# Kernel tuning notes

Measured on AMD Instinct MI355X. Metric: run time of the kernel, lower is better.

Reference implementation:

```python
import jax, jax.numpy as jnp
import numpy as np

MODS = ['linguistic', 'emotient', 'acoustic', 'image']
HID = {'linguistic': 128, 'emotient': 20, 'acoustic': 64, 'image': 128}
DIMS = {'linguistic': 300, 'emotient': 30, 'acoustic': 88, 'image': 1000}
B, T = 64, 512
TOTAL_HID = sum(HID[m] for m in MODS)  # 340
FUSE_HID = 64


def setup_inputs() -> dict:
    key = jax.random.key(0)
    ks = iter(jax.random.split(key, 64))
    inp = {}
    for mod in MODS:
        H, D = HID[mod], DIMS[mod]
        s = 1.0 / np.sqrt(H)
        inp[f'x_{mod}'] = jax.random.normal(next(ks), (B, T, D), jnp.float32)
        inp[f'present_{mod}'] = jax.random.randint(next(ks), (B, T), 0, 2).astype(jnp.int32)
        inp[f'W_ih_{mod}'] = jax.random.uniform(next(ks), (4 * H, D), jnp.float32, -s, s)
        inp[f'W_hh_{mod}'] = jax.random.uniform(next(ks), (4 * H, H), jnp.float32, -s, s)
        inp[f'b_ih_{mod}'] = jax.random.uniform(next(ks), (4 * H,), jnp.float32, -s, s)
        inp[f'b_hh_{mod}'] = jax.random.uniform(next(ks), (4 * H,), jnp.float32, -s, s)
    inp['seq_length'] = jax.random.randint(next(ks), (B,), 1, T + 1).astype(jnp.int32)
    valid = (jnp.arange(T)[None, :] < inp['seq_length'][:, None])
    inp['lstm_masks'] = valid.astype(jnp.float32)[:, :, None]
    s1 = 1.0 / np.sqrt(TOTAL_HID)
    inp['fuse_W1'] = jax.random.uniform(next(ks), (FUSE_HID, TOTAL_HID), jnp.float32, -s1, s1)
    inp['fuse_b1'] = jax.random.uniform(next(ks), (FUSE_HID,), jnp.float32, -s1, s1)
    s2 = 1.0 / np.sqrt(FUSE_HID)
    inp['fuse_W2'] = jax.random.uniform(next(ks), (1, FUSE_HID), jnp.float32, -s2, s2)
    inp['fuse_b2'] = jax.random.uniform(next(ks), (1,), jnp.float32, -s2, s2)
    return inp


def _lstm_scan(x, present, W_ih, W_hh, b_ih, b_hh):
    # x: [B,T,D], present: [B,T] in {0,1}. Carries (h,c) when not present (async arrival).
    Bn, Tn, _ = x.shape
    H = W_hh.shape[1]
    xg = jnp.einsum('btd,gd->btg', x, W_ih) + b_ih  # [B,T,4H] batched input GEMM

    def step(carry, inp):
        h, c = carry
        xg_t, p_t = inp  # [B,4H], [B]
        g = xg_t + h @ W_hh.T + b_hh
        i, f, gg, o = jnp.split(g, 4, axis=-1)
        i, f, o = jax.nn.sigmoid(i), jax.nn.sigmoid(f), jax.nn.sigmoid(o)
        gg = jnp.tanh(gg)
        c_new = f * c + i * gg
        h_new = o * jnp.tanh(c_new)
        p = p_t[:, None].astype(h.dtype)
        h2 = p * h_new + (1.0 - p) * h
        c2 = p * c_new + (1.0 - p) * c
        return (h2, c2), h2

    init = (jnp.zeros((Bn, H), x.dtype), jnp.zeros((Bn, H), x.dtype))
    _, hs = jax.lax.scan(step, init, (jnp.swapaxes(xg, 0, 1), present.T))
    return jnp.swapaxes(hs, 0, 1)  # [B,T,H]


def reference(x_linguistic, x_emotient, x_acoustic, x_image,
              present_linguistic, present_emotient, present_acoustic, present_image,
              W_ih_linguistic, W_hh_linguistic, b_ih_linguistic, b_hh_linguistic,
              W_ih_emotient, W_hh_emotient, b_ih_emotient, b_hh_emotient,
              W_ih_acoustic, W_hh_acoustic, b_ih_acoustic, b_hh_acoustic,
              W_ih_image, W_hh_image, b_ih_image, b_hh_image,
              seq_length, lstm_masks, fuse_W1, fuse_b1, fuse_W2, fuse_b2):
    xs = {'linguistic': x_linguistic, 'emotient': x_emotient, 'acoustic': x_acoustic, 'image': x_image}
    pres = {'linguistic': present_linguistic, 'emotient': present_emotient,
            'acoustic': present_acoustic, 'image': present_image}
    Wih = {'linguistic': W_ih_linguistic, 'emotient': W_ih_emotient, 'acoustic': W_ih_acoustic, 'image': W_ih_image}
    Whh = {'linguistic': W_hh_linguistic, 'emotient': W_hh_emotient, 'acoustic': W_hh_acoustic, 'image': W_hh_image}
    bih = {'linguistic': b_ih_linguistic, 'emotient': b_ih_emotient, 'acoustic': b_ih_acoustic, 'image': b_ih_image}
    bhh = {'linguistic': b_hh_linguistic, 'emotient': b_hh_emotient, 'acoustic': b_hh_acoustic, 'image': b_hh_image}
    hs = [_lstm_scan(xs[m], pres[m], Wih[m], Whh[m], bih[m], bhh[m]) for m in MODS]
    h = jnp.concatenate(hs, axis=-1)  # [B,T,340]
    # padded timesteps past seq_length are zeros in the original (zeros appended)
    valid = (jnp.arange(h.shape[1])[None, :] < seq_length[:, None]).astype(h.dtype)
    h = h * valid[:, :, None]
    out = h @ fuse_W1.T + fuse_b1  # Dropout is identity at inference
    out = out @ fuse_W2.T + fuse_b2
    return out * lstm_masks
```

## Files before the change

kernel.cpp:

```cpp
#include <hip/hip_runtime.h>
#include <stdint.h>

typedef __bf16 bf16_t;
typedef _Float16 fp16_t;
typedef bf16_t bf16x8 __attribute__((ext_vector_type(8)));
typedef fp16_t fp16x4 __attribute__((ext_vector_type(4)));
typedef float f32x4 __attribute__((ext_vector_type(4)));

#define LOG2E 1.44269504088896340736f

__device__ __forceinline__ float sigm(float x) {
    return __builtin_amdgcn_rcpf(1.f + __builtin_amdgcn_exp2f(-LOG2E * x));
}
__device__ __forceinline__ float tanh_(float x) {
    return 1.f - 2.f * __builtin_amdgcn_rcpf(1.f + __builtin_amdgcn_exp2f((2.f * LOG2E) * x));
}

template <int CTRL>
__device__ __forceinline__ float dpp_add(float x) {
    int perm = __builtin_amdgcn_update_dpp(0, __float_as_int(x), CTRL, 0xF, 0xF, true);
    return x + __int_as_float(perm);
}
__device__ __forceinline__ float red16(float x) {
    x = dpp_add<0xB1>(x);
    x = dpp_add<0x4E>(x);
    x = dpp_add<0x124>(x);
    x = dpp_add<0x128>(x);
    return x;
}

__global__ void prep_fuse(const float* __restrict__ W1, const float* __restrict__ b1,
                          const float* __restrict__ W2, const float* __restrict__ b2,
                          float* __restrict__ v) {
    int u = threadIdx.x;
    if (u < 340) {
        float s = 0.f;
        for (int j = 0; j < 64; j++) s += W2[j] * W1[j * 340 + u];
        v[u] = s;
    } else if (u == 340) {
        float s = 0.f;
        for (int j = 0; j < 64; j++) s += W2[j] * b1[j];
        v[340] = s + b2[0];
    }
}

struct ModGemm {
    const float* x; const float* w; const float* bih; const float* bhh; fp16_t* xg;
    int D; int KB; int N4; int hshift;
};
struct GemmArgs { ModGemm m[4]; int slot_mi[11]; int slot_nb[11]; };

__global__ __launch_bounds__(512) void gemm_all(GemmArgs ga) {
    __shared__ bf16_t sAh[256 * 40];
    __shared__ bf16_t sAl[256 * 40];
    __shared__ bf16_t sB[128 * 40];
    const int slot = blockIdx.y;
    const ModGemm mg = ga.m[ga.slot_mi[slot]];
    const int nb = ga.slot_nb[slot];
    const int ncol0 = nb << 7;
    const int tid = threadIdx.x;
    const int w = tid >> 6, l = tid & 63, lm = l & 15, q = l >> 4;
    const int wm = w & 3, wn = w >> 2;
    const int bm = blockIdx.x;
    const int D = mg.D, N4 = mg.N4;
    const int ra = tid >> 1, ca = (tid & 1) << 4;
    const int rb = tid >> 2, cb = (tid & 3) << 3;

    f32x4 acc[4][4];
#pragma unroll
    for (int a = 0; a < 4; a++)
#pragma unroll
        for (int b = 0; b < 4; b++) acc[a][b] = 0.f;

    for (int kb = 0; kb < mg.KB; kb++) {
        const int k0 = kb << 5;
        {
            long grow = (long)(bm << 8) + ra;
            const float* src = mg.x + grow * D + k0 + ca;
            union { bf16_t e[16]; bf16x8 v[2]; } uh, ul;
            if (k0 + ca + 16 <= D) {
#pragma unroll
                for (int j = 0; j < 16; j += 2) {
                    float2 f = *(const float2*)(src + j);
                    bf16_t h0 = (bf16_t)f.x, h1 = (bf16_t)f.y;
                    uh.e[j] = h0; uh.e[j + 1] = h1;
                    ul.e[j] = (bf16_t)(f.x - (float)h0);
                    ul.e[j + 1] = (bf16_t)(f.y - (float)h1);
                }
            } else {
#pragma unroll
                for (int j = 0; j < 16; j++) {
                    int k = k0 + ca + j;
                    float fv = (k < D) ? mg.x[grow * D + k] : 0.f;
                    bf16_t h0 = (bf16_t)fv;
                    uh.e[j] = h0; ul.e[j] = (bf16_t)(fv - (float)h0);
                }
            }
            *(bf16x8*)&sAh[ra * 40 + ca] = uh.v[0];
            *(bf16x8*)&sAh[ra * 40 + ca + 8] = uh.v[1];
            *(bf16x8*)&sAl[ra * 40 + ca] = ul.v[0];
            *(bf16x8*)&sAl[ra * 40 + ca + 8] = ul.v[1];
        }
        {
            int wrow = ncol0 + rb;
            bool vr = wrow < N4;
            const float* src = mg.w + (long)wrow * D + k0 + cb;
            union { bf16_t e[8]; bf16x8 v; } ub;
            if (vr && (k0 + cb + 8 <= D)) {
#pragma unroll
                for (int j = 0; j < 8; j += 2) {
                    float2 f = *(const float2*)(src + j);
                    ub.e[j] = (bf16_t)f.x; ub.e[j + 1] = (bf16_t)f.y;
                }
            } else {
#pragma unroll
                for (int j = 0; j < 8; j++) {
                    int k = k0 + cb + j;
                    ub.e[j] = (vr && k < D) ? (bf16_t)mg.w[(long)wrow * D + k] : (bf16_t)0.f;
                }
            }
            *(bf16x8*)&sB[rb * 40 + cb] = ub.v;
        }
        __syncthreads();
        bf16x8 ah[4], al[4];
#pragma unroll
        for (int mt = 0; mt < 4; mt++) {
            int row = (wm << 6) + (mt << 4) + lm;
            ah[mt] = *(const bf16x8*)&sAh[row * 40 + (q << 3)];
            al[mt] = *(const bf16x8*)&sAl[row * 40 + (q << 3)];
        }
#pragma unroll
        for (int nt = 0; nt < 4; nt++) {
            bf16x8 bfv = *(const bf16x8*)&sB[((wn << 6) + (nt << 4) + lm) * 40 + (q << 3)];
#pragma unroll
            for (int mt = 0; mt < 4; mt++) {
                acc[mt][nt] = __builtin_amdgcn_mfma_f32_16x16x32_bf16(ah[mt], bfv, acc[mt][nt], 0, 0, 0);
                acc[mt][nt] = __builtin_amdgcn_mfma_f32_16x16x32_bf16(al[mt], bfv, acc[mt][nt], 0, 0, 0);
            }
        }
        __syncthreads();
    }
#pragma unroll
    for (int nt = 0; nt < 4; nt++) {
        int col = ncol0 + (wn << 6) + (nt << 4) + lm;
        if (col >= N4) continue;
        float bias = mg.bih[col] + mg.bhh[col];
        int colout = mg.hshift ? ((col & ((1 << mg.hshift) - 1)) << 2) | (col >> mg.hshift) : col;
#pragma unroll
        for (int mt = 0; mt < 4; mt++) {
#pragma unroll
            for (int r = 0; r < 4; r++) {
                long row = (long)(bm << 8) + (wm << 6) + (mt << 4) + (q << 2) + r;
                int b = (int)(row >> 9), t = (int)(row & 511);
                size_t dst = ((size_t)(t << 6) + b) * N4 + colout;
                mg.xg[dst] = (fp16_t)(acc[mt][nt][r] + bias);
            }
        }
    }
}

struct ModRec {
    const float* whh; const int* present; const fp16_t* xg;
    int N4; int voff;
};
struct RecArgs {
    ModRec m[4];
    const float* vvec;
    float* s_out;
};

template <int H>
__device__ __forceinline__ void rec_step(
    int t, bool act, int w, int lm, int q, int b0,
    const bf16x8 (&wf)[4][H / 32], float vv,
    fp16x4 (&xvs)[4], const fp16_t* const (&px)[4], size_t tstride,
    float (&h_st)[4], float (&c_st)[4],
    const unsigned (&pw)[4], const bf16_t* __restrict__ hbR,
    bf16_t* __restrict__ hbW, float* __restrict__ s_out) {
    constexpr int KT = H / 32, Hp = H + 8;
    if (act) {
        bf16x8 af[KT];
#pragma unroll
        for (int kt = 0; kt < KT; kt++)
            af[kt] = *(const bf16x8*)&hbR[lm * Hp + (kt << 5) + (q << 3)];
        f32x4 accv[4];
#pragma unroll
        for (int g = 0; g < 4; g++)
#pragma unroll
            for (int r = 0; r < 4; r++)
                accv[g][r] = (float)xvs[r][g];
        int tn = t + 4;
        if (tn < 512) {
#pragma unroll
            for (int r = 0; r < 4; r++)
                xvs[r] = *(const fp16x4*)(px[r] + (size_t)tn * tstride);
        }
#pragma unroll
        for (int kt = 0; kt < KT; kt++)
#pragma unroll
            for (int g = 0; g < 4; g++)
                accv[g] = __builtin_amdgcn_mfma_f32_16x16x32_bf16(af[kt], wf[g][kt], accv[g], 0, 0, 0);
        float cr[4];
#pragma unroll
        for (int r = 0; r < 4; r++) {
            float gi = sigm(accv[0][r]);
            float gf = sigm(accv[1][r]);
            float gg = tanh_(accv[2][r]);
            float go = sigm(accv[3][r]);
            float cn = gf * c_st[r] + gi * gg;
            float hn = go * tanh_(cn);
            bool pb = ((pw[r] >> (t & 31)) & 1u) != 0u;
            h_st[r] = pb ? hn : h_st[r];
            c_st[r] = pb ? cn : c_st[r];
            cr[r] = h_st[r] * vv;
        }
        const int u = (w << 4) + lm;
#pragma unroll
        for (int r = 0; r < 4; r++)
            hbW[((q << 2) + r) * Hp + u] = (bf16_t)h_st[r];
#pragma unroll
        for (int r = 0; r < 4; r++)
            cr[r] = red16(cr[r]);
        if (lm == 0) {
#pragma unroll
            for (int r = 0; r < 4; r++)
                s_out[(size_t)((w << 6) + b0 + (q << 2) + r) * 512 + t] = cr[r];
        }
    }
    __syncthreads();
}

template <int H>
__device__ void rec_mfma(const ModRec M, int grp, float* __restrict__ s_out,
                         const float* __restrict__ vvec,
                         unsigned* presw, bf16_t* hb0, bf16_t* hb1, int tid) {
    constexpr int KT = H / 32, TPG = H / 16, Hp = H + 8;
    const int N4 = 4 * H;
    const int w = tid >> 6, l = tid & 63, lm = l & 15, q = l >> 4;
    const int b0 = grp << 4;
    const bool act = (w < TPG);

    for (int i = tid; i < 16 * Hp; i += 512) { hb0[i] = (bf16_t)0.f; hb1[i] = (bf16_t)0.f; }
    for (int i = tid; i < 256; i += 512) {
        const int* ps = M.present + ((b0 + (i >> 4)) << 9) + ((i & 15) << 5);
        unsigned bits = 0u;
#pragma unroll
        for (int j = 0; j < 32; j++) bits |= (unsigned)(ps[j] != 0) << j;
        presw[i] = bits;
    }

    bf16x8 wf[4][KT];
    float vv = 0.f;
    const int u = (w << 4) + lm;
    if (act) {
#pragma unroll
        for (int g = 0; g < 4; g++) {
            int n = g * H + u;
#pragma unroll
            for (int kt = 0; kt < KT; kt++) {
                int k = (kt << 5) + (q << 3);
                const float* sp_ = M.whh + (long)n * H + k;
                float4 f0 = *(const float4*)sp_;
                float4 f1 = *(const float4*)(sp_ + 4);
                union { bf16_t e[8]; bf16x8 v; } uu;
                uu.e[0] = (bf16_t)f0.x; uu.e[1] = (bf16_t)f0.y;
                uu.e[2] = (bf16_t)f0.z; uu.e[3] = (bf16_t)f0.w;
                uu.e[4] = (bf16_t)f1.x; uu.e[5] = (bf16_t)f1.y;
                uu.e[6] = (bf16_t)f1.z; uu.e[7] = (bf16_t)f1.w;
                wf[g][kt] = uu.v;
            }
        }
        vv = vvec[M.voff + u];
    }
    const fp16_t* px[4];
#pragma unroll
    for (int r = 0; r < 4; r++)
        px[r] = M.xg + (size_t)(b0 + (q << 2) + r) * N4 + (u << 2);
    const size_t tstride = (size_t)64 * N4;

    fp16x4 xv[4][4];
    if (act) {
#pragma unroll
        for (int s = 0; s < 4; s++)
#pragma unroll
            for (int r = 0; r < 4; r++)
                xv[s][r] = *(const fp16x4*)(px[r] + (size_t)s * tstride);
    }
    float h_st[4] = {0, 0, 0, 0}, c_st[4] = {0, 0, 0, 0};
    unsigned pw[4] = {0, 0, 0, 0};
    __syncthreads();

    for (int t0 = 0; t0 < 512; t0 += 4) {
        if ((t0 & 31) == 0 && act) {
            int wd = t0 >> 5;
#pragma unroll
            for (int r = 0; r < 4; r++)
                pw[r] = presw[(((q << 2) + r) << 4) + wd];
        }
        rec_step<H>(t0 + 0, act, w, lm, q, b0, wf, vv, xv[0], px, tstride, h_st, c_st, pw, hb0, hb1, s_out);
        rec_step<H>(t0 + 1, act, w, lm, q, b0, wf, vv, xv[1], px, tstride, h_st, c_st, pw, hb1, hb0, s_out);
        rec_step<H>(t0 + 2, act, w, lm, q, b0, wf, vv, xv[2], px, tstride, h_st, c_st, pw, hb0, hb1, s_out);
        rec_step<H>(t0 + 3, act, w, lm, q, b0, wf, vv, xv[3], px, tstride, h_st, c_st, pw, hb1, hb0, s_out);
    }
}

__device__ void rec_emot(const ModRec M, int grp, float* __restrict__ s_out,
                         const float* __restrict__ vvec,
                         float* presf, float* gbuf , float* he , int tid) {
    const int b0 = grp << 4;
    for (int i = tid; i < 16 * 21; i += 512) he[i] = 0.f;
    for (int i = tid; i < 16 * 512; i += 512)
        presf[i] = (float)M.present[((b0 + (i >> 9)) << 9) + (i & 511)];
    const int bl = tid >> 5;
    const int j0 = tid & 31;
    const bool has2 = (j0 < 16);
    float wr0[20], wr1[20], wr2[20];
#pragma unroll
    for (int k = 0; k < 20; k++) {
        wr0[k] = M.whh[j0 * 20 + k];
        wr1[k] = M.whh[(j0 + 32) * 20 + k];
        wr2[k] = has2 ? M.whh[(j0 + 64) * 20 + k] : 0.f;
    }
    const int b2 = tid / 20, u2 = tid % 20;
    const bool p2 = (tid < 320);
    float c_st = 0.f, h_st = 0.f;
    const fp16_t* px = M.xg + (size_t)(b0 + bl) * 80;
    fp16_t e0[4], e1[4], e2[4];
#pragma unroll
    for (int s = 0; s < 4; s++) {
        const fp16_t* p = px + (size_t)s * 5120;
        e0[s] = p[j0]; e1[s] = p[j0 + 32]; e2[s] = has2 ? p[j0 + 64] : (fp16_t)0.f;
    }
    __syncthreads();

    for (int t0 = 0; t0 < 512; t0 += 4) {
#pragma unroll
        for (int s = 0; s < 4; s++) {
            int t = t0 + s;
            float g0 = (float)e0[s];
            float g1 = (float)e1[s];
            float g2 = has2 ? (float)e2[s] : 0.f;
            int tn = t + 4;
            if (tn < 512) {
                const fp16_t* p = px + (size_t)tn * 5120;
                e0[s] = p[j0]; e1[s] = p[j0 + 32]; if (has2) e2[s] = p[j0 + 64];
            }
#pragma unroll
            for (int k = 0; k < 20; k++) {
                float hv = he[bl * 21 + k];
                g0 += wr0[k] * hv; g1 += wr1[k] * hv; g2 += wr2[k] * hv;
            }
            gbuf[bl * 81 + j0] = g0;
            gbuf[bl * 81 + j0 + 32] = g1;
            if (has2) gbuf[bl * 81 + j0 + 64] = g2;
            __syncthreads();
            if (p2) {
                float gi = sigm(gbuf[b2 * 81 + u2]);
                float gf = sigm(gbuf[b2 * 81 + u2 + 20]);
                float gg = tanh_(gbuf[b2 * 81 + u2 + 40]);
                float go = sigm(gbuf[b2 * 81 + u2 + 60]);
                float cn = gf * c_st + gi * gg;
                float hn = go * tanh_(cn);
                float p = presf[b2 * 512 + t];
                bool pb = (p != 0.f);
                h_st = pb ? hn : h_st;
                c_st = pb ? cn : c_st;
                he[b2 * 21 + u2] = h_st;
            }
            __syncthreads();
            if (tid < 16) {
                float ssum = 0.f;
#pragma unroll
                for (int uu = 0; uu < 20; uu++) ssum += he[tid * 21 + uu] * vvec[M.voff + uu];
                s_out[((b0 + tid) << 9) + t] = ssum;
            }
        }
    }
}

__global__ __launch_bounds__(512) void rec_all(RecArgs ra) {
    __shared__ float presf[16 * 512];
    __shared__ bf16_t hb0[16 * 136];
    __shared__ bf16_t hb1[16 * 136];
    __shared__ float gbuf[16 * 81];
    __shared__ float he[16 * 21];
    __shared__ unsigned presw[16 * 16];
    const int tid = threadIdx.x;
    const int bid = blockIdx.x;
    const int mi = bid >> 2, grp = bid & 3;
    const ModRec M = ra.m[mi];
    float* s_out = ra.s_out + (size_t)mi * 8 * 64 * 512;
    if (mi == 1)      rec_emot(M, grp, s_out, ra.vvec, presf, gbuf, he, tid);
    else if (mi == 2) rec_mfma<64>(M, grp, s_out, ra.vvec, presw, hb0, hb1, tid);
    else              rec_mfma<128>(M, grp, s_out, ra.vvec, presw, hb0, hb1, tid);
}

__global__ void fuse_out(const float* __restrict__ sp, const float* __restrict__ v,
                         const float* __restrict__ masks, float* __restrict__ out) {
    int i = threadIdx.x + blockIdx.x * 256;
    float c0 = v[340];
    float s = 0.f;
#pragma unroll
    for (int w = 0; w < 8; w++) s += sp[(size_t)w * 32768 + i];
    s += sp[(size_t)8 * 32768 + i];
#pragma unroll
    for (int w = 16; w < 20; w++) s += sp[(size_t)w * 32768 + i];
#pragma unroll
    for (int w = 24; w < 32; w++) s += sp[(size_t)w * 32768 + i];
    out[i] = masks[i] * (s + c0);
}

extern "C" void kernel_launch(void* const* d_in, const int* in_sizes, int n_in,
                              void* d_out, int out_size, void* d_ws, size_t ws_size,
                              hipStream_t stream) {
    const float* xL = (const float*)d_in[0];
    const int*   pL = (const int*)d_in[1];
    const float* WihL = (const float*)d_in[2];
    const float* WhhL = (const float*)d_in[3];
    const float* bihL = (const float*)d_in[4];
    const float* bhhL = (const float*)d_in[5];
    const float* xE = (const float*)d_in[6];
    const int*   pE = (const int*)d_in[7];
    const float* WihE = (const float*)d_in[8];
    const float* WhhE = (const float*)d_in[9];
    const float* bihE = (const float*)d_in[10];
    const float* bhhE = (const float*)d_in[11];
    const float* xA = (const float*)d_in[12];
    const int*   pA = (const int*)d_in[13];
    const float* WihA = (const float*)d_in[14];
    const float* WhhA = (const float*)d_in[15];
    const float* bihA = (const float*)d_in[16];
    const float* bhhA = (const float*)d_in[17];
    const float* xI = (const float*)d_in[18];
    const int*   pI = (const int*)d_in[19];
    const float* WihI = (const float*)d_in[20];
    const float* WhhI = (const float*)d_in[21];
    const float* bihI = (const float*)d_in[22];
    const float* bhhI = (const float*)d_in[23];
    const float* masks = (const float*)d_in[25];
    const float* fW1 = (const float*)d_in[26];
    const float* fb1 = (const float*)d_in[27];
    const float* fW2 = (const float*)d_in[28];
    const float* fb2 = (const float*)d_in[29];

    char* ws = (char*)d_ws;
    float* v     = (float*)ws;
    float* spart = (float*)(ws + (1 << 16));
    fp16_t* xgL = (fp16_t*)(ws + (1 << 16) + (4 << 20));
    fp16_t* xgE = xgL + (size_t)32768 * 512;
    fp16_t* xgA = xgE + (size_t)32768 * 80;
    fp16_t* xgI = xgA + (size_t)32768 * 256;

    prep_fuse<<<dim3(1), dim3(512), 0, stream>>>(fW1, fb1, fW2, fb2, v);

    GemmArgs ga;
    ga.m[0] = {xL, WihL, bihL, bhhL, xgL, 300,  10, 512, 7};
    ga.m[1] = {xE, WihE, bihE, bhhE, xgE, 30,   1,  80,  0};
    ga.m[2] = {xA, WihA, bihA, bhhA, xgA, 88,   3,  256, 6};
    ga.m[3] = {xI, WihI, bihI, bhhI, xgI, 1000, 32, 512, 7};
    const int mi_tab[11] = {0, 0, 0, 0, 3, 3, 3, 3, 2, 2, 1};
    const int nb_tab[11] = {0, 1, 2, 3, 0, 1, 2, 3, 0, 1, 0};
    for (int i = 0; i < 11; i++) { ga.slot_mi[i] = mi_tab[i]; ga.slot_nb[i] = nb_tab[i]; }
    gemm_all<<<dim3(128, 11), dim3(512), 0, stream>>>(ga);

    RecArgs ra;
    ra.m[0] = {WhhL, pL, xgL, 512, 0};
    ra.m[1] = {WhhE, pE, xgE, 80,  128};
    ra.m[2] = {WhhA, pA, xgA, 256, 148};
    ra.m[3] = {WhhI, pI, xgI, 512, 212};
    ra.vvec = v;
    ra.s_out = spart;
    rec_all<<<dim3(16), dim3(512), 0, stream>>>(ra);

    fuse_out<<<dim3(128), dim3(256), 0, stream>>>(spart, v, masks, (float*)d_out);
}
```

Measured before the change: 1.031 ms.

## Fuse input GEMM and LSTM recurrence into one persistent kernel with per-chunk flags

Merges the batched input-projection GEMM and the recurrent LSTM kernels into a single launch. The GEMM tiles are reordered to be time-major so each tile covers a 4-timestep chunk. Each finished tile bumps an atomic flag, and the 16 recurrence blocks spin on those flags chunk by chunk. This lets the serial recurrence start while later-timestep projections are still being computed, instead of waiting for the whole GEMM to finish. It adds spin-wait and acquire/release overhead every 4 steps. It also relies on the low-index recurrence blocks staying resident while the GEMM blocks make progress, which risks deadlock or stalls if scheduling differs.

New measurement: 1.030 ms. About the same (-0.1%).

```diff
diff --git a/kernel.cpp b/kernel.cpp
--- a/kernel.cpp
+++ b/kernel.cpp
@@ -27,6 +27,15 @@
     x = dpp_add<0x124>(x);
     x = dpp_add<0x128>(x);
     return x;
+}
+
+__device__ __forceinline__ void gate_chunk(const int* fp, int need, int tid) {
+    if ((tid >> 6) == 0) {
+        while (__hip_atomic_load(fp, __ATOMIC_RELAXED, __HIP_MEMORY_SCOPE_AGENT) < need)
+            __builtin_amdgcn_s_sleep(2);
+        (void)__hip_atomic_load(fp, __ATOMIC_ACQUIRE, __HIP_MEMORY_SCOPE_AGENT);
+    }
+    __syncthreads();
 }
 
 __global__ void prep_fuse(const float* __restrict__ W1, const float* __restrict__ b1,
@@ -48,20 +57,26 @@
     const float* x; const float* w; const float* bih; const float* bhh; fp16_t* xg;
     int D; int KB; int N4; int hshift;
 };
-struct GemmArgs { ModGemm m[4]; int slot_mi[11]; int slot_nb[11]; };
-
-__global__ __launch_bounds__(512) void gemm_all(GemmArgs ga) {
-    __shared__ bf16_t sAh[256 * 40];
-    __shared__ bf16_t sAl[256 * 40];
-    __shared__ bf16_t sB[128 * 40];
-    const int slot = blockIdx.y;
-    const ModGemm mg = ga.m[ga.slot_mi[slot]];
-    const int nb = ga.slot_nb[slot];
+struct ModRec {
+    const float* whh; const int* present; const fp16_t* xg;
+    int N4; int voff;
+};
+struct MegaArgs {
+    ModGemm gm[4];
+    int slot_mi[11]; int slot_nb[11];
+    ModRec rm[4];
+    const float* vvec;
+    float* s_out;
+    int* flags;
+    int need[4];
+};
+
+__device__ void gemm_body(const ModGemm mg, int nb, int bm, int mi,
+                          int* __restrict__ flags, int tid,
+                          bf16_t* sAh, bf16_t* sAl, bf16_t* sB) {
     const int ncol0 = nb << 7;
-    const int tid = threadIdx.x;
     const int w = tid >> 6, l = tid & 63, lm = l & 15, q = l >> 4;
     const int wm = w & 3, wn = w >> 2;
-    const int bm = blockIdx.x;
     const int D = mg.D, N4 = mg.N4;
     const int ra = tid >> 1, ca = (tid & 1) << 4;
     const int rb = tid >> 2, cb = (tid & 3) << 3;
@@ -75,8 +90,10 @@
     for (int kb = 0; kb < mg.KB; kb++) {
         const int k0 = kb << 5;
         {
-            long grow = (long)(bm << 8) + ra;
-            const float* src = mg.x + grow * D + k0 + ca;
+            long row = (long)(bm << 8) + ra;
+            int tt = (int)(row >> 6), bb = (int)(row & 63);
+            const float* base = mg.x + ((size_t)bb * 512 + tt) * D;
+            const float* src = base + k0 + ca;
             union { bf16_t e[16]; bf16x8 v[2]; } uh, ul;
             if (k0 + ca + 16 <= D) {
 #pragma unroll
@@ -91,7 +108,7 @@
 #pragma unroll
                 for (int j = 0; j < 16; j++) {
                     int k = k0 + ca + j;
-                    float fv = (k < D) ? mg.x[grow * D + k] : 0.f;
+                    float fv = (k < D) ? base[k] : 0.f;
                     bf16_t h0 = (bf16_t)fv;
                     uh.e[j] = h0; ul.e[j] = (bf16_t)(fv - (float)h0);
                 }
@@ -151,23 +168,17 @@
 #pragma unroll
             for (int r = 0; r < 4; r++) {
                 long row = (long)(bm << 8) + (wm << 6) + (mt << 4) + (q << 2) + r;
-                int b = (int)(row >> 9), t = (int)(row & 511);
-                size_t dst = ((size_t)(t << 6) + b) * N4 + colout;
-                mg.xg[dst] = (fp16_t)(acc[mt][nt][r] + bias);
-            }
-        }
-    }
-}
-
-struct ModRec {
-    const float* whh; const int* present; const fp16_t* xg;
-    int N4; int voff;
-};
-struct RecArgs {
-    ModRec m[4];
-    const float* vvec;
-    float* s_out;
-};
+                mg.xg[(size_t)row * N4 + colout] = (fp16_t)(acc[mt][nt][r] + bias);
+            }
+        }
+    }
+    __syncthreads();
+    if (tid == 0) {
+        __threadfence();
+        __hip_atomic_fetch_add(&flags[mi * 128 + bm], 1, __ATOMIC_RELEASE,
+                               __HIP_MEMORY_SCOPE_AGENT);
+    }
+}
 
 template <int H>
 __device__ __forceinline__ void rec_step(
@@ -233,6 +244,7 @@
 template <int H>
 __device__ void rec_mfma(const ModRec M, int grp, float* __restrict__ s_out,
                          const float* __restrict__ vvec,
+                         const int* __restrict__ flagp, int need,
                          unsigned* presw, bf16_t* hb0, bf16_t* hb1, int tid) {
     constexpr int KT = H / 32, TPG = H / 16, Hp = H + 8;
     const int N4 = 4 * H;
@@ -278,6 +290,8 @@
         px[r] = M.xg + (size_t)(b0 + (q << 2) + r) * N4 + (u << 2);
     const size_t tstride = (size_t)64 * N4;
 
+    gate_chunk(flagp, need, tid);
+
     fp16x4 xv[4][4];
     if (act) {
 #pragma unroll
@@ -291,6 +305,8 @@
     __syncthreads();
 
     for (int t0 = 0; t0 < 512; t0 += 4) {
+        int cn = (t0 >> 2) + 1;
+        if (cn < 128) gate_chunk(flagp + cn, need, tid);
         if ((t0 & 31) == 0 && act) {
             int wd = t0 >> 5;
 #pragma unroll
@@ -306,6 +322,7 @@
 
 __device__ void rec_emot(const ModRec M, int grp, float* __restrict__ s_out,
                          const float* __restrict__ vvec,
+                         const int* __restrict__ flagp, int need,
                          float* presf, float* gbuf , float* he , int tid) {
     const int b0 = grp << 4;
     for (int i = tid; i < 16 * 21; i += 512) he[i] = 0.f;
@@ -325,6 +342,9 @@
     const bool p2 = (tid < 320);
     float c_st = 0.f, h_st = 0.f;
     const fp16_t* px = M.xg + (size_t)(b0 + bl) * 80;
+
+    gate_chunk(flagp, need, tid);
+
     fp16_t e0[4], e1[4], e2[4];
 #pragma unroll
     for (int s = 0; s < 4; s++) {
@@ -334,6 +354,8 @@
     __syncthreads();
 
     for (int t0 = 0; t0 < 512; t0 += 4) {
+        int cn = (t0 >> 2) + 1;
+        if (cn < 128) gate_chunk(flagp + cn, need, tid);
 #pragma unroll
         for (int s = 0; s < 4; s++) {
             int t = t0 + s;
@@ -359,12 +381,12 @@
                 float gf = sigm(gbuf[b2 * 81 + u2 + 20]);
                 float gg = tanh_(gbuf[b2 * 81 + u2 + 40]);
                 float go = sigm(gbuf[b2 * 81 + u2 + 60]);
-                float cn = gf * c_st + gi * gg;
-                float hn = go * tanh_(cn);
+                float cn2 = gf * c_st + gi * gg;
+                float hn = go * tanh_(cn2);
                 float p = presf[b2 * 512 + t];
                 bool pb = (p != 0.f);
                 h_st = pb ? hn : h_st;
-                c_st = pb ? cn : c_st;
+                c_st = pb ? cn2 : c_st;
                 he[b2 * 21 + u2] = h_st;
             }
             __syncthreads();
@@ -378,21 +400,35 @@
     }
 }
 
-__global__ __launch_bounds__(512) void rec_all(RecArgs ra) {
-    __shared__ float presf[16 * 512];
-    __shared__ bf16_t hb0[16 * 136];
-    __shared__ bf16_t hb1[16 * 136];
-    __shared__ float gbuf[16 * 81];
-    __shared__ float he[16 * 21];
-    __shared__ unsigned presw[16 * 16];
+__global__ __launch_bounds__(512) void mega(MegaArgs A) {
+    __shared__ __align__(16) char smem[51712];
     const int tid = threadIdx.x;
     const int bid = blockIdx.x;
-    const int mi = bid >> 2, grp = bid & 3;
-    const ModRec M = ra.m[mi];
-    float* s_out = ra.s_out + (size_t)mi * 8 * 64 * 512;
-    if (mi == 1)      rec_emot(M, grp, s_out, ra.vvec, presf, gbuf, he, tid);
-    else if (mi == 2) rec_mfma<64>(M, grp, s_out, ra.vvec, presw, hb0, hb1, tid);
-    else              rec_mfma<128>(M, grp, s_out, ra.vvec, presw, hb0, hb1, tid);
+    if (bid < 16) {
+        float*    presf = (float*)smem;
+        bf16_t*   hb0   = (bf16_t*)(smem + 32768);
+        bf16_t*   hb1   = (bf16_t*)(smem + 37120);
+        float*    gbuf  = (float*)(smem + 41472);
+        float*    he    = (float*)(smem + 46656);
+        unsigned* presw = (unsigned*)(smem + 48000);
+        const int mi = bid >> 2, grp = bid & 3;
+        const ModRec M = A.rm[mi];
+        const int* flagp = A.flags + mi * 128;
+        const int need = A.need[mi];
+        float* s_out = A.s_out + (size_t)mi * 8 * 64 * 512;
+        if (mi == 1)      rec_emot(M, grp, s_out, A.vvec, flagp, need, presf, gbuf, he, tid);
+        else if (mi == 2) rec_mfma<64>(M, grp, s_out, A.vvec, flagp, need, presw, hb0, hb1, tid);
+        else              rec_mfma<128>(M, grp, s_out, A.vvec, flagp, need, presw, hb0, hb1, tid);
+    } else {
+        bf16_t* sAh = (bf16_t*)smem;
+        bf16_t* sAl = (bf16_t*)(smem + 20480);
+        bf16_t* sB  = (bf16_t*)(smem + 40960);
+        int e = bid - 16;
+        int bmi = e / 11;
+        int slot = e - bmi * 11;
+        int mi = A.slot_mi[slot];
+        gemm_body(A.gm[mi], A.slot_nb[slot], bmi, mi, A.flags, tid, sAh, sAl, sB);
+    }
 }
 
 __global__ void fuse_out(const float* __restrict__ sp, const float* __restrict__ v,
@@ -445,6 +481,7 @@
 
     char* ws = (char*)d_ws;
     float* v     = (float*)ws;
+    int*   flags = (int*)(ws + 4096);
     float* spart = (float*)(ws + (1 << 16));
     fp16_t* xgL = (fp16_t*)(ws + (1 << 16) + (4 << 20));
     fp16_t* xgE = xgL + (size_t)32768 * 512;
@@ -452,25 +489,26 @@
     fp16_t* xgI = xgA + (size_t)32768 * 256;
 
     prep_fuse<<<dim3(1), dim3(512), 0, stream>>>(fW1, fb1, fW2, fb2, v);
-
-    GemmArgs ga;
-    ga.m[0] = {xL, WihL, bihL, bhhL, xgL, 300,  10, 512, 7};
-    ga.m[1] = {xE, WihE, bihE, bhhE, xgE, 30,   1,  80,  0};
-    ga.m[2] = {xA, WihA, bihA, bhhA, xgA, 88,   3,  256, 6};
-    ga.m[3] = {xI, WihI, bihI, bhhI, xgI, 1000, 32, 512, 7};
+    hipMemsetAsync(flags, 0, 4 * 128 * sizeof(int), stream);
+
+    MegaArgs A;
+    A.gm[0] = {xL, WihL, bihL, bhhL, xgL, 300,  10, 512, 7};
+    A.gm[1] = {xE, WihE, bihE, bhhE, xgE, 30,   1,  80,  0};
+    A.gm[2] = {xA, WihA, bihA, bhhA, xgA, 88,   3,  256, 6};
+    A.gm[3] = {xI, WihI, bihI, bhhI, xgI, 1000, 32, 512, 7};
     const int mi_tab[11] = {0, 0, 0, 0, 3, 3, 3, 3, 2, 2, 1};
     const int nb_tab[11] = {0, 1, 2, 3, 0, 1, 2, 3, 0, 1, 0};
-    for (int i = 0; i < 11; i++) { ga.slot_mi[i] = mi_tab[i]; ga.slot_nb[i] = nb_tab[i]; }
-    gemm_all<<<dim3(128, 11), dim3(512), 0, stream>>>(ga);
-
-    RecArgs ra;
-    ra.m[0] = {WhhL, pL, xgL, 512, 0};
-    ra.m[1] = {WhhE, pE, xgE, 80,  128};
-    ra.m[2] = {WhhA, pA, xgA, 256, 148};
-    ra.m[3] = {WhhI, pI, xgI, 512, 212};
-    ra.vvec = v;
-    ra.s_out = spart;
-    rec_all<<<dim3(16), dim3(512), 0, stream>>>(ra);
+    for (int i = 0; i < 11; i++) { A.slot_mi[i] = mi_tab[i]; A.slot_nb[i] = nb_tab[i]; }
+    A.rm[0] = {WhhL, pL, xgL, 512, 0};
+    A.rm[1] = {WhhE, pE, xgE, 80,  128};
+    A.rm[2] = {WhhA, pA, xgA, 256, 148};
+    A.rm[3] = {WhhI, pI, xgI, 512, 212};
+    A.vvec = v;
+    A.s_out = spart;
+    A.flags = flags;
+    A.need[0] = 4; A.need[1] = 1; A.need[2] = 2; A.need[3] = 4;
+
+    mega<<<dim3(16 + 128 * 11), dim3(512), 0, stream>>>(A);
 
     fuse_out<<<dim3(128), dim3(256), 0, stream>>>(spart, v, masks, (float*)d_out);
 }
```
